# Kernel optimization log

Measured on AMD Instinct MI355X. Metric: run time of the kernel, lower is better.

## Reference

```python
import jax, jax.numpy as jnp
import numpy as np


def setup_inputs() -> dict:
    key = jax.random.key(0)
    k1, k2 = jax.random.split(key)
    B, S, D, H = 64, 2048, 128, 128
    x = jax.random.normal(k1, (B, S, D), dtype=jnp.float32)
    # net = Linear(D+H -> H) + tanh; torch Linear default init scale ~ 1/sqrt(fan_in)
    W = jax.random.normal(k2, (D + H, H), dtype=jnp.float32) / np.sqrt(D + H)
    b = jnp.zeros((H,), dtype=jnp.float32)
    return {"x": x, "W": W, "b": b}


def reference(x, W, b):
    B, S, D = x.shape
    H = W.shape[1]
    # Split W so we avoid materializing concat(x_t, hidden) each step:
    # net(cat(x_t, h)) = tanh(x_t @ Wx + h @ Wh + b)
    Wx, Wh = W[:D], W[D:]
    # Precompute the input projection for all timesteps in one big GEMM.
    xproj = jnp.einsum("bsd,dh->bsh", x, Wx) + b  # [B, S, H]

    h0 = jnp.zeros((B, H), dtype=x.dtype)

    def step(h, xp_t):
        h_new = jnp.tanh(xp_t + h @ Wh)
        return h_new, h_new

    # scan over time: xproj transposed to [S, B, H]
    hidden, outputs = jax.lax.scan(step, h0, jnp.swapaxes(xproj, 0, 1))
    outputs = jnp.swapaxes(outputs, 0, 1)  # [B, S, H]
    return outputs, hidden
```

## Files before the change

kernel.cpp:

```cpp
#include <hip/hip_runtime.h>

#define BB 64
#define SS 2048
#define DD 128
#define HH 128

typedef float v2f __attribute__((ext_vector_type(2)));

#define PKBLO(acc, hp, w) \
    asm("v_pk_fma_f32 %0, %1, %2, %0 op_sel_hi:[0,1,1]" \
        : "+v"(acc) : "v"(hp), "v"(w))
#define PKBHI(acc, hp, w) \
    asm("v_pk_fma_f32 %0, %1, %2, %0 op_sel:[1,0,0] op_sel_hi:[1,1,1]" \
        : "+v"(acc) : "v"(hp), "v"(w))

#define LDW(var, r, u) { \
    const float* _p = Whp + (long)(32 * s + kr##r * 4 + (u)) * HH + j0; \
    asm volatile("global_load_dwordx2 %0, %1, off" : "=&v"(var) : "v"(_p)); }

__device__ __forceinline__ float fast_tanh(float x) {
    float e = __expf(2.0f * x);
    return 1.0f - __fdividef(2.0f, e + 1.0f);
}

__device__ __forceinline__ float quad_allreduce(float v) {
    int a = __builtin_amdgcn_update_dpp(0, __float_as_int(v), 0xB1, 0xF, 0xF, true);
    v += __int_as_float(a);
    int c = __builtin_amdgcn_update_dpp(0, __float_as_int(v), 0x4E, 0xF, 0xF, true);
    v += __int_as_float(c);
    return v;
}

__device__ __forceinline__ void wg_sync_lds() {
    asm volatile("s_waitcnt lgkmcnt(0)\n\ts_barrier" ::: "memory");
}

__global__ __launch_bounds__(256, 2)
void xproj_kernel(const float* __restrict__ x, const float* __restrict__ W,
                  const float* __restrict__ bias, float* __restrict__ out) {
    __shared__ __align__(16) float4 wxs[64 * 32];
    __shared__ __align__(16) float4 xsw[128 * 16];
    const int tid = threadIdx.x;
    const int tx  = tid & 15;
    const int ty  = tid >> 4;
    const long row0 = (long)blockIdx.x * 128;

    float acc[8][8];
#pragma unroll
    for (int i = 0; i < 8; ++i)
#pragma unroll
        for (int j = 0; j < 8; ++j) acc[i][j] = 0.f;

    for (int kh = 0; kh < 2; ++kh) {
        {
            const float4* wg = (const float4*)(W + kh * 64 * HH);
#pragma unroll
            for (int i = 0; i < 8; ++i) wxs[tid + i * 256] = wg[tid + i * 256];
        }
        {
#pragma unroll
            for (int i = 0; i < 8; ++i) {
                const int g  = tid + i * 256;
                const int r  = g >> 4;
                const int k4 = g & 15;
                const float4 v = ((const float4*)(x + (row0 + r) * DD + kh * 64))[k4];
                xsw[r * 16 + (k4 ^ ((r >> 3) & 7))] = v;
            }
        }
        __syncthreads();

        for (int k4 = 0; k4 < 16; ++k4) {
            float4 xa[8];
#pragma unroll
            for (int i = 0; i < 8; ++i)
                xa[i] = xsw[(ty * 8 + i) * 16 + (k4 ^ (ty & 7))];
            float4 wa[4][2];
#pragma unroll
            for (int kk = 0; kk < 4; ++kk) {
                wa[kk][0] = wxs[(k4 * 4 + kk) * 32 + tx * 2];
                wa[kk][1] = wxs[(k4 * 4 + kk) * 32 + tx * 2 + 1];
            }
#pragma unroll
            for (int i = 0; i < 8; ++i) {
#pragma unroll
                for (int kk = 0; kk < 4; ++kk) {
                    const float xv = (kk == 0) ? xa[i].x : (kk == 1) ? xa[i].y
                                   : (kk == 2) ? xa[i].z : xa[i].w;
                    acc[i][0] = fmaf(xv, wa[kk][0].x, acc[i][0]);
                    acc[i][1] = fmaf(xv, wa[kk][0].y, acc[i][1]);
                    acc[i][2] = fmaf(xv, wa[kk][0].z, acc[i][2]);
                    acc[i][3] = fmaf(xv, wa[kk][0].w, acc[i][3]);
                    acc[i][4] = fmaf(xv, wa[kk][1].x, acc[i][4]);
                    acc[i][5] = fmaf(xv, wa[kk][1].y, acc[i][5]);
                    acc[i][6] = fmaf(xv, wa[kk][1].z, acc[i][6]);
                    acc[i][7] = fmaf(xv, wa[kk][1].w, acc[i][7]);
                }
            }
        }
        __syncthreads();
    }

    const float4 b0 = ((const float4*)bias)[tx * 2];
    const float4 b1 = ((const float4*)bias)[tx * 2 + 1];
#pragma unroll
    for (int i = 0; i < 8; ++i) {
        const float4 o0 = make_float4(acc[i][0] + b0.x, acc[i][1] + b0.y,
                                      acc[i][2] + b0.z, acc[i][3] + b0.w);
        const float4 o1 = make_float4(acc[i][4] + b1.x, acc[i][5] + b1.y,
                                      acc[i][6] + b1.z, acc[i][7] + b1.w);
        float4* og = (float4*)(out + (row0 + ty * 8 + i) * HH);
        og[tx * 2]     = o0;
        og[tx * 2 + 1] = o1;
    }
}

__global__ __launch_bounds__(256, 1)
void rnn_kernel(const float* __restrict__ W, float* __restrict__ out) {
    const int CH = 16;
    const int NC = SS / CH;

    __shared__ __align__(16) float hb[2][HH];

    const int b    = blockIdx.x;
    const int tid  = threadIdx.x;
    const int w    = tid >> 6;
    const int lane = tid & 63;
    const int s    = lane & 3;
    const int jj   = lane >> 2;
    const int j0   = w * 32 + 2 * jj;

    const int kr0 = (0 + 2 * s) & 7, kr1 = (1 + 2 * s) & 7;
    const int kr2 = (2 + 2 * s) & 7, kr3 = (3 + 2 * s) & 7;
    const int kr4 = (4 + 2 * s) & 7, kr5 = (5 + 2 * s) & 7;
    const int kr6 = (6 + 2 * s) & 7, kr7 = (7 + 2 * s) & 7;

    const float* Whp = W + (long)DD * HH;

    v2f w00, w01, w02, w03, w10, w11, w12, w13;
    v2f w20, w21, w22, w23, w30, w31, w32, w33;
    v2f w40, w41, w42, w43, w50, w51, w52, w53;
    v2f w60, w61, w62, w63, w70, w71, w72, w73;
    LDW(w00,0,0) LDW(w01,0,1) LDW(w02,0,2) LDW(w03,0,3)
    LDW(w10,1,0) LDW(w11,1,1) LDW(w12,1,2) LDW(w13,1,3)
    LDW(w20,2,0) LDW(w21,2,1) LDW(w22,2,2) LDW(w23,2,3)
    LDW(w30,3,0) LDW(w31,3,1) LDW(w32,3,2) LDW(w33,3,3)
    LDW(w40,4,0) LDW(w41,4,1) LDW(w42,4,2) LDW(w43,4,3)
    LDW(w50,5,0) LDW(w51,5,1) LDW(w52,5,2) LDW(w53,5,3)
    LDW(w60,6,0) LDW(w61,6,1) LDW(w62,6,2) LDW(w63,6,3)
    LDW(w70,7,0) LDW(w71,7,1) LDW(w72,7,2) LDW(w73,7,3)

    float* const xbase = out + (long)b * SS * HH;

    if (tid < 128) { hb[0][tid] = 0.f; hb[1][tid] = 0.f; }

    v2f xpc[4], nxt[4];
    {
        const float* g0 = xbase + (4 * s) * HH + j0;
        const float* g1 = xbase + (CH + 4 * s) * HH + j0;
#pragma unroll
        for (int i = 0; i < 4; ++i) { xpc[i] = *(const v2f*)(g0 + i * HH);
                                      nxt[i] = *(const v2f*)(g1 + i * HH); }
    }
    asm volatile("s_waitcnt vmcnt(0)" ::: "memory");
    wg_sync_lds();

    for (int c = 0; c < NC; ++c) {
#pragma unroll
        for (int tt = 0; tt < CH; ++tt) {
            const int t = c * CH + tt;
            const float4* hv = (const float4*)hb[(t + 1) & 1];

            v2f P0 = {0.f, 0.f}, P1 = {0.f, 0.f};
            v2f P2 = {0.f, 0.f}, P3 = {0.f, 0.f};
#define STEP_R(r) { \
            const float4 h4 = hv[8 * s + kr##r]; \
            v2f hlo; hlo.x = h4.x; hlo.y = h4.y; \
            v2f hhi; hhi.x = h4.z; hhi.y = h4.w; \
            PKBLO(P0, hlo, w##r##0); \
            PKBHI(P1, hlo, w##r##1); \
            PKBLO(P2, hhi, w##r##2); \
            PKBHI(P3, hhi, w##r##3); }
            STEP_R(0) STEP_R(1) STEP_R(2) STEP_R(3)
            STEP_R(4) STEP_R(5) STEP_R(6) STEP_R(7)
#undef STEP_R
            const v2f P = (P0 + P1) + (P2 + P3);
            float fA = P.x, fB = P.y;
            const bool own = (s == (tt >> 2));
            fA += own ? xpc[tt & 3].x : 0.f;
            fB += own ? xpc[tt & 3].y : 0.f;
            fA = quad_allreduce(fA);
            fB = quad_allreduce(fB);

            const float h = fast_tanh((s < 2) ? fA : fB);
            const int col = j0 + (s >> 1);
            if ((s & 1) == 0) hb[t & 1][col] = h;
            else              xbase[(long)t * HH + col] = h;
            wg_sync_lds();
        }
        if (c + 1 < NC) {
#pragma unroll
            for (int i = 0; i < 4; ++i) xpc[i] = nxt[i];
            if (c + 2 < NC) {
                const float* g = xbase + ((long)(c + 2) * CH + 4 * s) * HH + j0;
#pragma unroll
                for (int i = 0; i < 4; ++i) nxt[i] = *(const v2f*)(g + i * HH);
            }
        }
    }

    if (tid < 128) {
        out[(long)BB * SS * HH + b * HH + tid] = hb[1][tid];
    }
}

extern "C" void kernel_launch(void* const* d_in, const int* in_sizes, int n_in,
                              void* d_out, int out_size, void* d_ws, size_t ws_size,
                              hipStream_t stream) {
    const float* x    = (const float*)d_in[0];
    const float* W    = (const float*)d_in[1];
    const float* bias = (const float*)d_in[2];
    float* out = (float*)d_out;

    xproj_kernel<<<dim3((BB * SS) / 128), dim3(256), 0, stream>>>(x, W, bias, out);
    rnn_kernel<<<dim3(BB), dim3(256), 0, stream>>>(W, out);
}
```

Before: 733.4 us.

## Halve RNN block to 128 threads, each thread computing four hidden columns

The recurrent kernel now runs with 2 waves instead of 4. Each quad of lanes covers four output columns, so each thread holds twice as many Wh registers (64 v2f) and issues twice the packed FMAs per step. Each thread then owns exactly one hidden element for both the LDS write and the global write, and xproj is preloaded per thread as 16 scalars. The aim is to cut barrier cost and wave-synchronisation overhead on the serial per-step critical path, at the cost of longer per-thread FMA chains and higher register pressure.

```diff
diff --git a/kernel.cpp b/kernel.cpp
--- a/kernel.cpp
+++ b/kernel.cpp
@@ -14,9 +14,10 @@
     asm("v_pk_fma_f32 %0, %1, %2, %0 op_sel:[1,0,0] op_sel_hi:[1,1,1]" \
         : "+v"(acc) : "v"(hp), "v"(w))
 
-#define LDW(var, r, u) { \
-    const float* _p = Whp + (long)(32 * s + kr##r * 4 + (u)) * HH + j0; \
-    asm volatile("global_load_dwordx2 %0, %1, off" : "=&v"(var) : "v"(_p)); }
+#define LDA(r, u) asm volatile("global_load_dwordx2 %0, %1, off" \
+    : "=&v"(a##r##u) : "v"(Whp + (long)(32 * s + kr##r * 4 + (u)) * HH + j0));
+#define LDB(r, u) asm volatile("global_load_dwordx2 %0, %1, off" \
+    : "=&v"(b##r##u) : "v"(Whp + (long)(32 * s + kr##r * 4 + (u)) * HH + j0 + 2));
 
 __device__ __forceinline__ float fast_tanh(float x) {
     float e = __expf(2.0f * x);
@@ -114,53 +115,54 @@
     }
 }
 
-__global__ __launch_bounds__(256, 1)
+__global__ __launch_bounds__(128, 1) __attribute__((amdgpu_waves_per_eu(1, 1)))
 void rnn_kernel(const float* __restrict__ W, float* __restrict__ out) {
     const int CH = 16;
     const int NC = SS / CH;
 
     __shared__ __align__(16) float hb[2][HH];
 
-    const int b    = blockIdx.x;
-    const int tid  = threadIdx.x;
-    const int w    = tid >> 6;
-    const int lane = tid & 63;
-    const int s    = lane & 3;
-    const int jj   = lane >> 2;
-    const int j0   = w * 32 + 2 * jj;
+    const int b   = blockIdx.x;
+    const int tid = threadIdx.x;
+    const int w   = tid >> 6;
+    const int l   = tid & 63;
+    const int s   = l & 3;
+    const int j0  = 64 * w + 4 * (l >> 2);
 
     const int kr0 = (0 + 2 * s) & 7, kr1 = (1 + 2 * s) & 7;
     const int kr2 = (2 + 2 * s) & 7, kr3 = (3 + 2 * s) & 7;
     const int kr4 = (4 + 2 * s) & 7, kr5 = (5 + 2 * s) & 7;
     const int kr6 = (6 + 2 * s) & 7, kr7 = (7 + 2 * s) & 7;
+    const int ix0 = 8 * s + kr0, ix1 = 8 * s + kr1, ix2 = 8 * s + kr2,
+              ix3 = 8 * s + kr3, ix4 = 8 * s + kr4, ix5 = 8 * s + kr5,
+              ix6 = 8 * s + kr6, ix7 = 8 * s + kr7;
 
     const float* Whp = W + (long)DD * HH;
 
-    v2f w00, w01, w02, w03, w10, w11, w12, w13;
-    v2f w20, w21, w22, w23, w30, w31, w32, w33;
-    v2f w40, w41, w42, w43, w50, w51, w52, w53;
-    v2f w60, w61, w62, w63, w70, w71, w72, w73;
-    LDW(w00,0,0) LDW(w01,0,1) LDW(w02,0,2) LDW(w03,0,3)
-    LDW(w10,1,0) LDW(w11,1,1) LDW(w12,1,2) LDW(w13,1,3)
-    LDW(w20,2,0) LDW(w21,2,1) LDW(w22,2,2) LDW(w23,2,3)
-    LDW(w30,3,0) LDW(w31,3,1) LDW(w32,3,2) LDW(w33,3,3)
-    LDW(w40,4,0) LDW(w41,4,1) LDW(w42,4,2) LDW(w43,4,3)
-    LDW(w50,5,0) LDW(w51,5,1) LDW(w52,5,2) LDW(w53,5,3)
-    LDW(w60,6,0) LDW(w61,6,1) LDW(w62,6,2) LDW(w63,6,3)
-    LDW(w70,7,0) LDW(w71,7,1) LDW(w72,7,2) LDW(w73,7,3)
+    v2f a00,a01,a02,a03, a10,a11,a12,a13, a20,a21,a22,a23, a30,a31,a32,a33;
+    v2f a40,a41,a42,a43, a50,a51,a52,a53, a60,a61,a62,a63, a70,a71,a72,a73;
+    v2f b00,b01,b02,b03, b10,b11,b12,b13, b20,b21,b22,b23, b30,b31,b32,b33;
+    v2f b40,b41,b42,b43, b50,b51,b52,b53, b60,b61,b62,b63, b70,b71,b72,b73;
+    LDA(0,0) LDA(0,1) LDA(0,2) LDA(0,3)  LDB(0,0) LDB(0,1) LDB(0,2) LDB(0,3)
+    LDA(1,0) LDA(1,1) LDA(1,2) LDA(1,3)  LDB(1,0) LDB(1,1) LDB(1,2) LDB(1,3)
+    LDA(2,0) LDA(2,1) LDA(2,2) LDA(2,3)  LDB(2,0) LDB(2,1) LDB(2,2) LDB(2,3)
+    LDA(3,0) LDA(3,1) LDA(3,2) LDA(3,3)  LDB(3,0) LDB(3,1) LDB(3,2) LDB(3,3)
+    LDA(4,0) LDA(4,1) LDA(4,2) LDA(4,3)  LDB(4,0) LDB(4,1) LDB(4,2) LDB(4,3)
+    LDA(5,0) LDA(5,1) LDA(5,2) LDA(5,3)  LDB(5,0) LDB(5,1) LDB(5,2) LDB(5,3)
+    LDA(6,0) LDA(6,1) LDA(6,2) LDA(6,3)  LDB(6,0) LDB(6,1) LDB(6,2) LDB(6,3)
+    LDA(7,0) LDA(7,1) LDA(7,2) LDA(7,3)  LDB(7,0) LDB(7,1) LDB(7,2) LDB(7,3)
 
     float* const xbase = out + (long)b * SS * HH;
 
-    if (tid < 128) { hb[0][tid] = 0.f; hb[1][tid] = 0.f; }
-
-    v2f xpc[4], nxt[4];
-    {
-        const float* g0 = xbase + (4 * s) * HH + j0;
-        const float* g1 = xbase + (CH + 4 * s) * HH + j0;
-#pragma unroll
-        for (int i = 0; i < 4; ++i) { xpc[i] = *(const v2f*)(g0 + i * HH);
-                                      nxt[i] = *(const v2f*)(g1 + i * HH); }
-    }
+    hb[0][tid] = 0.f;
+    hb[1][tid] = 0.f;
+
+    float xpc[16], nxt[16];
+#pragma unroll
+    for (int i = 0; i < 16; ++i) xpc[i] = xbase[(long)i * HH + tid];
+#pragma unroll
+    for (int i = 0; i < 16; ++i) nxt[i] = xbase[(long)(CH + i) * HH + tid];
+
     asm volatile("s_waitcnt vmcnt(0)" ::: "memory");
     wg_sync_lds();
 
@@ -170,47 +172,48 @@
             const int t = c * CH + tt;
             const float4* hv = (const float4*)hb[(t + 1) & 1];
 
-            v2f P0 = {0.f, 0.f}, P1 = {0.f, 0.f};
-            v2f P2 = {0.f, 0.f}, P3 = {0.f, 0.f};
+            v2f p0 = {0.f,0.f}, p1 = {0.f,0.f}, p2 = {0.f,0.f}, p3 = {0.f,0.f};
+            v2f q0 = {0.f,0.f}, q1 = {0.f,0.f}, q2 = {0.f,0.f}, q3 = {0.f,0.f};
 #define STEP_R(r) { \
-            const float4 h4 = hv[8 * s + kr##r]; \
+            const float4 h4 = hv[ix##r]; \
             v2f hlo; hlo.x = h4.x; hlo.y = h4.y; \
             v2f hhi; hhi.x = h4.z; hhi.y = h4.w; \
-            PKBLO(P0, hlo, w##r##0); \
-            PKBHI(P1, hlo, w##r##1); \
-            PKBLO(P2, hhi, w##r##2); \
-            PKBHI(P3, hhi, w##r##3); }
+            PKBLO(p0, hlo, a##r##0); PKBLO(q0, hlo, b##r##0); \
+            PKBHI(p1, hlo, a##r##1); PKBHI(q1, hlo, b##r##1); \
+            PKBLO(p2, hhi, a##r##2); PKBLO(q2, hhi, b##r##2); \
+            PKBHI(p3, hhi, a##r##3); PKBHI(q3, hhi, b##r##3); }
             STEP_R(0) STEP_R(1) STEP_R(2) STEP_R(3)
             STEP_R(4) STEP_R(5) STEP_R(6) STEP_R(7)
 #undef STEP_R
-            const v2f P = (P0 + P1) + (P2 + P3);
-            float fA = P.x, fB = P.y;
-            const bool own = (s == (tt >> 2));
-            fA += own ? xpc[tt & 3].x : 0.f;
-            fB += own ? xpc[tt & 3].y : 0.f;
-            fA = quad_allreduce(fA);
-            fB = quad_allreduce(fB);
-
-            const float h = fast_tanh((s < 2) ? fA : fB);
-            const int col = j0 + (s >> 1);
-            if ((s & 1) == 0) hb[t & 1][col] = h;
-            else              xbase[(long)t * HH + col] = h;
+            const v2f P = (p0 + p1) + (p2 + p3);
+            const v2f Q = (q0 + q1) + (q2 + q3);
+
+            const float rpx = quad_allreduce(P.x);
+            const float rpy = quad_allreduce(P.y);
+            const float rqx = quad_allreduce(Q.x);
+            const float rqy = quad_allreduce(Q.y);
+
+            const float e0 = (s & 1) ? rpy : rpx;
+            const float e1 = (s & 1) ? rqy : rqx;
+            const float hx = ((s & 2) ? e1 : e0) + xpc[tt];
+            const float h  = fast_tanh(hx);
+
+            hb[t & 1][tid] = h;
+            xbase[(long)t * HH + tid] = h;
             wg_sync_lds();
         }
         if (c + 1 < NC) {
 #pragma unroll
-            for (int i = 0; i < 4; ++i) xpc[i] = nxt[i];
+            for (int i = 0; i < 16; ++i) xpc[i] = nxt[i];
             if (c + 2 < NC) {
-                const float* g = xbase + ((long)(c + 2) * CH + 4 * s) * HH + j0;
-#pragma unroll
-                for (int i = 0; i < 4; ++i) nxt[i] = *(const v2f*)(g + i * HH);
+                const float* g = xbase + (long)(c + 2) * CH * HH + tid;
+#pragma unroll
+                for (int i = 0; i < 16; ++i) nxt[i] = g[(long)i * HH];
             }
         }
     }
 
-    if (tid < 128) {
-        out[(long)BB * SS * HH + b * HH + tid] = hb[1][tid];
-    }
+    out[(long)BB * SS * HH + b * HH + tid] = hb[(SS - 1) & 1][tid];
 }
 
 extern "C" void kernel_launch(void* const* d_in, const int* in_sizes, int n_in,
@@ -222,5 +225,5 @@
     float* out = (float*)d_out;
 
     xproj_kernel<<<dim3((BB * SS) / 128), dim3(256), 0, stream>>>(x, W, bias, out);
-    rnn_kernel<<<dim3(BB), dim3(256), 0, stream>>>(W, out);
-}
+    rnn_kernel<<<dim3(BB), dim3(128), 0, stream>>>(W, out);
+}
```

Result: slower. 812.3 us (+10.8%).
